# Kernel optimization log

Measured on AMD Instinct MI355X. Metric: run time of the kernel, lower is better.

## Reference

```python
import jax, jax.numpy as jnp
import numpy as np

B, N, F = 2, 3000, 64
H, OUT, ATT = 4, 16, 16
DENSITY = 0.01


def setup_inputs() -> dict:
    key = jax.random.key(0)
    ks = jax.random.split(key, 6)
    h = jax.random.normal(ks[0], (B, N, F), dtype=jnp.float32)
    a = (jax.random.uniform(ks[1], (B, N, N)) < DENSITY).astype(jnp.float32)
    glorot = lambda k, shape: jax.random.uniform(
        k, shape, jnp.float32, -1.0, 1.0) * jnp.sqrt(6.0 / (shape[-2] + shape[-1]))
    kernel = glorot(ks[2], (H, F, OUT))
    attention_kernel = glorot(ks[3], (H, F, ATT))
    attention_kernel_2 = glorot(ks[4], (H, F, ATT))
    bias = jax.random.normal(ks[5], (1, 1, H, OUT), dtype=jnp.float32) * 0.01
    return {"h": h, "a": a, "kernel": kernel,
            "attention_kernel": attention_kernel,
            "attention_kernel_2": attention_kernel_2, "bias": bias}


def reference(h, a, kernel, attention_kernel, attention_kernel_2, bias):
    # h: [B,N,F], a: [B,N,N] dense binary adjacency
    feats = jnp.einsum('bnf,hfo->bhno', h, kernel)            # [B,H,N,OUT]
    f_self = jnp.einsum('bnf,hfd->hbnd', h, attention_kernel)   # [H,B,N,A]
    f_other = jnp.einsum('bnf,hfd->hbdn', h, attention_kernel_2)  # [H,B,A,N]
    a_h = a[None]                                               # [1,B,N,N] broadcast over heads
    scores = jnp.einsum('hbnd,hbdm->hbnm', f_self, f_other)     # [H,B,N,N]
    masked = a_h * scores
    masked = jnp.where(masked >= 0, masked, 0.2 * masked)       # LeakyReLU(0.2)
    masked = masked / jnp.sqrt(jnp.float32(ATT))
    masked = masked + jnp.where(a_h == 0, jnp.float32(-1e9), jnp.float32(0.0))
    attn = jax.nn.softmax(masked, axis=-1)
    attn = attn * jnp.where(a_h == 0, jnp.float32(0.0), jnp.float32(1.0))
    attn = jnp.transpose(attn, (1, 0, 2, 3))                    # [B,H,N,N]
    # dropout_rate=0 / inference -> identity
    node_features = jnp.einsum('bhnm,bhmo->bhno', attn, feats)  # [B,H,N,OUT]
    node_features = node_features + jnp.transpose(bias, (0, 2, 1, 3))  # [1,H,1,OUT]
    node_features = jax.nn.relu(node_features)
    node_features = jnp.transpose(node_features, (0, 2, 1, 3))  # [B,N,H,OUT]
    return node_features.reshape(-1, N, H * OUT)
```

## Files before the change

kernel.cpp:

```cpp
#include <hip/hip_runtime.h>
#include <math.h>

#define B_   2
#define N_   3000
#define F_   64
#define H_   4
#define O_   16
#define HO_  64
#define MAXD 64
#define NF4  750
#define NN   (B_*N_)
#define NPB  12

typedef float f32x4 __attribute__((ext_vector_type(4)));

template<int CTRL>
__device__ __forceinline__ float ror_add(float x) {
    const int r = __builtin_amdgcn_update_dpp(0, __float_as_int(x), CTRL, 0xF, 0xF, true);
    return x + __int_as_float(r);
}
__device__ __forceinline__ float seg16_sum(float x) {
    x = ror_add<0x121>(x);
    x = ror_add<0x122>(x);
    x = ror_add<0x124>(x);
    x = ror_add<0x128>(x);
    return x;
}

__global__ __launch_bounds__(192) void proj_kernel(
    const float* __restrict__ h,
    const float* __restrict__ K,
    const float* __restrict__ AK,
    const float* __restrict__ AK2,
    float* __restrict__ comb,
    float* __restrict__ fs)
{
    const int tid  = threadIdx.x;
    const int m    = tid >> 6;
    const int lane = tid & 63;
    const int nbase = blockIdx.x * NPB;

    __shared__ float4 hrow[NPB][16];

    {
        const int j  = tid >> 4;
        const int f4 = tid & 15;
        hrow[j][f4] = ((const float4*)(h + (size_t)(nbase + j) * F_))[f4];
    }

    const float* Wm = (m == 0) ? AK2 : (m == 1) ? K : AK;
    const float* Wc = Wm + ((lane >> 4) << 10) + (lane & 15);
    f32x4 w4[16];
#pragma unroll
    for (int f4 = 0; f4 < 16; ++f4) {
        w4[f4][0] = Wc[(f4 * 4 + 0) << 4];
        w4[f4][1] = Wc[(f4 * 4 + 1) << 4];
        w4[f4][2] = Wc[(f4 * 4 + 2) << 4];
        w4[f4][3] = Wc[(f4 * 4 + 3) << 4];
    }
    __syncthreads();

#pragma unroll
    for (int j = 0; j < NPB; ++j) {
        float a0 = 0.f, a1 = 0.f, a2 = 0.f, a3 = 0.f;
#pragma unroll
        for (int f4 = 0; f4 < 16; ++f4) {
            const float4 hv = hrow[j][f4];
            a0 = fmaf(hv.x, w4[f4][0], a0);
            a1 = fmaf(hv.y, w4[f4][1], a1);
            a2 = fmaf(hv.z, w4[f4][2], a2);
            a3 = fmaf(hv.w, w4[f4][3], a3);
        }
        const float av = (a0 + a1) + (a2 + a3);
        const int node = nbase + j;
        if (m == 0)      comb[(size_t)node * 128 + lane]      = av;
        else if (m == 1) comb[(size_t)node * 128 + 64 + lane] = av;
        else             fs  [(size_t)node * HO_ + lane]      = av;
    }
}

__global__ __launch_bounds__(256, 8) void gat_wave_kernel(
    const float* __restrict__ a,
    const float* __restrict__ comb,
    const float* __restrict__ fs,
    const float* __restrict__ bias,
    float* __restrict__ out)
{
    const int tid  = threadIdx.x;
    const int w    = tid >> 6;
    const int lane = tid & 63;
    const int row  = blockIdx.x * 4 + w;
    const int b    = row / N_;
    const int bbase = b * N_;

    __shared__ int nbr[4][MAXD];

    const float biasv = bias[lane];
    const float fsv   = fs[(size_t)row * HO_ + lane];

    const f32x4* arow = (const f32x4*)(a + (size_t)row * N_);
    unsigned long long msk = 0ull;
#pragma unroll
    for (int g = 0; g < 3; ++g) {
        f32x4 v[4];
#pragma unroll
        for (int it = 0; it < 4; ++it) {
            const int c4 = (g * 4 + it) * 64 + lane;
            v[it] = (f32x4)(0.f);
            if (c4 < NF4) v[it] = arow[c4];
        }
#pragma unroll
        for (int it = 0; it < 4; ++it) {
            const unsigned int nib = (unsigned int)(v[it][0] != 0.f)
                                   | ((unsigned int)(v[it][1] != 0.f) << 1)
                                   | ((unsigned int)(v[it][2] != 0.f) << 2)
                                   | ((unsigned int)(v[it][3] != 0.f) << 3);
            msk |= ((unsigned long long)nib) << ((g * 4 + it) * 4);
        }
    }

    const int c = __popcll(msk);
    int incl = c;
#pragma unroll
    for (int d = 1; d < 64; d <<= 1) {
        const int t = __shfl_up(incl, d);
        if (lane >= d) incl += t;
    }
    int tot = __shfl(incl, 63);
    if (tot > MAXD) tot = MAXD;
    {
        unsigned long long m2 = msk;
        int k = incl - c;
        while (m2 && k < MAXD) {
            const int bpos = __builtin_ctzll(m2);
            m2 &= m2 - 1ull;
            nbr[w][k] = ((bpos >> 2) << 8) + (lane << 2) + (bpos & 3);
            ++k;
        }
    }
    asm volatile("s_waitcnt lgkmcnt(0)" ::: "memory");
    int nid = nbr[w][lane];
    nid = (lane < tot) ? nid : 0;

    float acc = 0.f, sum = 0.f;
#pragma unroll
    for (int bi = 0; bi < 16; ++bi) {
        if (bi * 4 < tot) {
            float fov[4], fev[4];
#pragma unroll
            for (int k = 0; k < 4; ++k) {
                const int m = __builtin_amdgcn_readlane(nid, bi * 4 + k);
                const float* bp = comb + ((size_t)(bbase + m) << 7);
                fov[k] = bp[lane];
                fev[k] = bp[64 + lane];
            }
            float s[4];
#pragma unroll
            for (int k = 0; k < 4; ++k) s[k] = seg16_sum(fsv * fov[k]);
#pragma unroll
            for (int k = 0; k < 4; ++k) {
                float t = (s[k] >= 0.f ? s[k] : 0.2f * s[k]) * 0.25f;
                const float e = (bi * 4 + k < tot) ? __expf(t) : 0.f;
                acc = fmaf(e, fev[k], acc);
                sum += e;
            }
        }
    }

    const float inv = (tot > 0) ? 1.f / sum : 0.f;
    out[(size_t)row * HO_ + lane] = fmaxf(fmaf(acc, inv, biasv), 0.f);
}

extern "C" void kernel_launch(void* const* d_in, const int* in_sizes, int n_in,
                              void* d_out, int out_size, void* d_ws, size_t ws_size,
                              hipStream_t stream) {
    const float* h    = (const float*)d_in[0];
    const float* a    = (const float*)d_in[1];
    const float* K    = (const float*)d_in[2];
    const float* AK   = (const float*)d_in[3];
    const float* AK2  = (const float*)d_in[4];
    const float* bias = (const float*)d_in[5];
    float* out = (float*)d_out;

    float* comb = (float*)d_ws;
    float* fs   = comb + (size_t)B_ * N_ * 128;

    hipLaunchKernelGGL(proj_kernel, dim3(NN / NPB), dim3(192), 0, stream,
                       h, K, AK, AK2, comb, fs);
    hipLaunchKernelGGL(gat_wave_kernel, dim3(B_ * N_ / 4), dim3(256), 0, stream,
                       a, comb, fs, bias, out);
}
```

Measured before the change: 35.50 us.

## Split adjacency bitmask extraction into a separate streaming kernel

Moves the dense adjacency scan out of the attention kernel into its own kernel. The new kernel reads the matrix with nontemporal loads and writes a compact per-row 64-bit mask array to workspace. The attention kernel then loads one mask word per lane instead of streaming 12 KB per row. This separates the bandwidth-bound scan from the latency-bound gather so each can keep more loads in flight, at the cost of an extra launch and a small extra write and read of the masks.

```diff
diff --git a/kernel.cpp b/kernel.cpp
--- a/kernel.cpp
+++ b/kernel.cpp
@@ -79,8 +79,32 @@
     }
 }
 
+__global__ __launch_bounds__(256) void bitmask_kernel(
+    const float* __restrict__ a,
+    unsigned long long* __restrict__ bm)
+{
+    const int w    = threadIdx.x >> 6;
+    const int lane = threadIdx.x & 63;
+    const int row  = blockIdx.x * 4 + w;
+    const f32x4* arow = (const f32x4*)(a + (size_t)row * N_);
+
+    unsigned long long msk = 0ull;
+#pragma unroll
+    for (int it = 0; it < 12; ++it) {
+        const int c4 = it * 64 + lane;
+        f32x4 v = (f32x4)(0.f);
+        if (c4 < NF4) v = __builtin_nontemporal_load(arow + c4);
+        const unsigned int nib = (unsigned int)(v[0] != 0.f)
+                               | ((unsigned int)(v[1] != 0.f) << 1)
+                               | ((unsigned int)(v[2] != 0.f) << 2)
+                               | ((unsigned int)(v[3] != 0.f) << 3);
+        msk |= ((unsigned long long)nib) << (it * 4);
+    }
+    bm[(size_t)row * 64 + lane] = msk;
+}
+
 __global__ __launch_bounds__(256, 8) void gat_wave_kernel(
-    const float* __restrict__ a,
+    const unsigned long long* __restrict__ bm,
     const float* __restrict__ comb,
     const float* __restrict__ fs,
     const float* __restrict__ bias,
@@ -97,27 +121,7 @@
 
     const float biasv = bias[lane];
     const float fsv   = fs[(size_t)row * HO_ + lane];
-
-    const f32x4* arow = (const f32x4*)(a + (size_t)row * N_);
-    unsigned long long msk = 0ull;
-#pragma unroll
-    for (int g = 0; g < 3; ++g) {
-        f32x4 v[4];
-#pragma unroll
-        for (int it = 0; it < 4; ++it) {
-            const int c4 = (g * 4 + it) * 64 + lane;
-            v[it] = (f32x4)(0.f);
-            if (c4 < NF4) v[it] = arow[c4];
-        }
-#pragma unroll
-        for (int it = 0; it < 4; ++it) {
-            const unsigned int nib = (unsigned int)(v[it][0] != 0.f)
-                                   | ((unsigned int)(v[it][1] != 0.f) << 1)
-                                   | ((unsigned int)(v[it][2] != 0.f) << 2)
-                                   | ((unsigned int)(v[it][3] != 0.f) << 3);
-            msk |= ((unsigned long long)nib) << ((g * 4 + it) * 4);
-        }
-    }
+    const unsigned long long msk = bm[(size_t)row * 64 + lane];
 
     const int c = __popcll(msk);
     int incl = c;
@@ -183,10 +187,14 @@
     float* out = (float*)d_out;
 
     float* comb = (float*)d_ws;
-    float* fs   = comb + (size_t)B_ * N_ * 128;
+    float* fs   = comb + (size_t)NN * 128;
+    unsigned long long* bmask =
+        (unsigned long long*)(fs + (size_t)NN * HO_);
 
     hipLaunchKernelGGL(proj_kernel, dim3(NN / NPB), dim3(192), 0, stream,
                        h, K, AK, AK2, comb, fs);
-    hipLaunchKernelGGL(gat_wave_kernel, dim3(B_ * N_ / 4), dim3(256), 0, stream,
-                       a, comb, fs, bias, out);
-}
+    hipLaunchKernelGGL(bitmask_kernel, dim3(NN / 4), dim3(256), 0, stream,
+                       a, bmask);
+    hipLaunchKernelGGL(gat_wave_kernel, dim3(NN / 4), dim3(256), 0, stream,
+                       bmask, comb, fs, bias, out);
+}
```

Result: slower. 40.68 us (+14.6%).

## Interleave neighbor feature pairs and batch gathers by sixteen with nontemporal adjacency loads

Applied to the files above, without the earlier changes.

The projection kernel now writes the f_other and feats values for each lane as an adjacent pair, so the aggregation kernel fetches both with a single 8-byte load per neighbor. Neighbor gathers are batched 16 at a time to put more loads in flight. Adjacency rows are read in two groups of six vectors using nontemporal loads to avoid polluting the cache. The occupancy hint in launch bounds is lowered from 8 to 4 to leave room for the extra live registers, which may reduce latency hiding and adds wasted work when a row has few neighbors.

```diff
diff --git a/kernel.cpp b/kernel.cpp
--- a/kernel.cpp
+++ b/kernel.cpp
@@ -13,6 +13,7 @@
 #define NPB  12
 
 typedef float f32x4 __attribute__((ext_vector_type(4)));
+typedef float f32x2 __attribute__((ext_vector_type(2)));
 
 template<int CTRL>
 __device__ __forceinline__ float ror_add(float x) {
@@ -32,7 +33,7 @@
     const float* __restrict__ K,
     const float* __restrict__ AK,
     const float* __restrict__ AK2,
-    float* __restrict__ comb,
+    float* __restrict__ combI,
     float* __restrict__ fs)
 {
     const int tid  = threadIdx.x;
@@ -73,15 +74,15 @@
         }
         const float av = (a0 + a1) + (a2 + a3);
         const int node = nbase + j;
-        if (m == 0)      comb[(size_t)node * 128 + lane]      = av;
-        else if (m == 1) comb[(size_t)node * 128 + 64 + lane] = av;
-        else             fs  [(size_t)node * HO_ + lane]      = av;
+        if (m == 0)      combI[(size_t)node * 128 + lane * 2 + 0] = av;
+        else if (m == 1) combI[(size_t)node * 128 + lane * 2 + 1] = av;
+        else             fs   [(size_t)node * HO_ + lane]         = av;
     }
 }
 
-__global__ __launch_bounds__(256, 8) void gat_wave_kernel(
+__global__ __launch_bounds__(256, 4) void gat_wave_kernel(
     const float* __restrict__ a,
-    const float* __restrict__ comb,
+    const float* __restrict__ combI,
     const float* __restrict__ fs,
     const float* __restrict__ bias,
     float* __restrict__ out)
@@ -101,21 +102,21 @@
     const f32x4* arow = (const f32x4*)(a + (size_t)row * N_);
     unsigned long long msk = 0ull;
 #pragma unroll
-    for (int g = 0; g < 3; ++g) {
-        f32x4 v[4];
+    for (int g = 0; g < 2; ++g) {
+        f32x4 v[6];
 #pragma unroll
-        for (int it = 0; it < 4; ++it) {
-            const int c4 = (g * 4 + it) * 64 + lane;
+        for (int it = 0; it < 6; ++it) {
+            const int c4 = (g * 6 + it) * 64 + lane;
             v[it] = (f32x4)(0.f);
-            if (c4 < NF4) v[it] = arow[c4];
+            if (c4 < NF4) v[it] = __builtin_nontemporal_load(arow + c4);
         }
 #pragma unroll
-        for (int it = 0; it < 4; ++it) {
+        for (int it = 0; it < 6; ++it) {
             const unsigned int nib = (unsigned int)(v[it][0] != 0.f)
                                    | ((unsigned int)(v[it][1] != 0.f) << 1)
                                    | ((unsigned int)(v[it][2] != 0.f) << 2)
                                    | ((unsigned int)(v[it][3] != 0.f) << 3);
-            msk |= ((unsigned long long)nib) << ((g * 4 + it) * 4);
+            msk |= ((unsigned long long)nib) << ((g * 6 + it) * 4);
         }
     }
 
@@ -143,29 +144,31 @@
     nid = (lane < tot) ? nid : 0;
 
     float acc = 0.f, sum = 0.f;
-#pragma unroll
-    for (int bi = 0; bi < 16; ++bi) {
-        if (bi * 4 < tot) {
-            float fov[4], fev[4];
-#pragma unroll
-            for (int k = 0; k < 4; ++k) {
-                const int m = __builtin_amdgcn_readlane(nid, bi * 4 + k);
-                const float* bp = comb + ((size_t)(bbase + m) << 7);
-                fov[k] = bp[lane];
-                fev[k] = bp[64 + lane];
-            }
-            float s[4];
-#pragma unroll
-            for (int k = 0; k < 4; ++k) s[k] = seg16_sum(fsv * fov[k]);
-#pragma unroll
-            for (int k = 0; k < 4; ++k) {
-                float t = (s[k] >= 0.f ? s[k] : 0.2f * s[k]) * 0.25f;
-                const float e = (bi * 4 + k < tot) ? __expf(t) : 0.f;
-                acc = fmaf(e, fev[k], acc);
-                sum += e;
-            }
-        }
+#define BATCH16(B0)                                                             \
+    {                                                                           \
+        f32x2 v[16];                                                            \
+        _Pragma("unroll")                                                       \
+        for (int k = 0; k < 16; ++k) {                                          \
+            const int mm = __builtin_amdgcn_readlane(nid, (B0) + k);            \
+            const f32x2* bp = (const f32x2*)(combI + ((size_t)(bbase + mm) << 7)); \
+            v[k] = bp[lane];                        \
+        }                                                                       \
+        _Pragma("unroll")                                                       \
+        for (int k = 0; k < 16; ++k) {                                          \
+            const float sdot = seg16_sum(fsv * v[k][0]);                        \
+            const float tt = (sdot >= 0.f ? sdot : 0.2f * sdot) * 0.25f;        \
+            const float e = ((B0) + k < tot) ? __expf(tt) : 0.f;                \
+            acc = fmaf(e, v[k][1], acc);                                        \
+            sum += e;                                                           \
+        }                                                                       \
     }
+    BATCH16(0);
+    if (tot > 16) BATCH16(16);
+    if (tot > 32) {
+        BATCH16(32);
+        if (tot > 48) BATCH16(48);
+    }
+#undef BATCH16
 
     const float inv = (tot > 0) ? 1.f / sum : 0.f;
     out[(size_t)row * HO_ + lane] = fmaxf(fmaf(acc, inv, biasv), 0.f);
@@ -182,11 +185,11 @@
     const float* bias = (const float*)d_in[5];
     float* out = (float*)d_out;
 
-    float* comb = (float*)d_ws;
-    float* fs   = comb + (size_t)B_ * N_ * 128;
+    float* combI = (float*)d_ws;
+    float* fs    = combI + (size_t)NN * 128;
 
     hipLaunchKernelGGL(proj_kernel, dim3(NN / NPB), dim3(192), 0, stream,
-                       h, K, AK, AK2, comb, fs);
-    hipLaunchKernelGGL(gat_wave_kernel, dim3(B_ * N_ / 4), dim3(256), 0, stream,
-                       a, comb, fs, bias, out);
+                       h, K, AK, AK2, combI, fs);
+    hipLaunchKernelGGL(gat_wave_kernel, dim3(NN / 4), dim3(256), 0, stream,
+                       a, combI, fs, bias, out);
 }
```

Result: no change. 35.80 us (+0.8%).
